# Kernel optimization log

Hardware: AMD Instinct MI355X
Metric: run time of the kernel (lower is better)

## Reference

```python
import jax, jax.numpy as jnp
import numpy as np

B, S, D = 4, 2048, 1024
H = 16
HD = D // H  # 64
MASKED_BIAS = jnp.float32(-10000.0)


def setup_inputs() -> dict:
    key = jax.random.key(0)
    ks = jax.random.split(key, 5)
    std = 0.02
    return {
        "hidden_states": jax.random.normal(ks[0], (B, S, D), jnp.float32),
        "Wq": jax.random.normal(ks[1], (D, D), jnp.float32) * std,
        "bq": jnp.zeros((D,), jnp.float32),
        "Wk": jax.random.normal(ks[2], (D, D), jnp.float32) * std,
        "bk": jnp.zeros((D,), jnp.float32),
        "Wv": jax.random.normal(ks[3], (D, D), jnp.float32) * std,
        "bv": jnp.zeros((D,), jnp.float32),
        "Wo": jax.random.normal(ks[4], (D, D), jnp.float32) * std,
        "bo": jnp.zeros((D,), jnp.float32),
    }


def _split_heads(x):
    # [B, S, D] -> [B, H, S, HD]
    return x.reshape(B, S, H, HD).transpose(0, 2, 1, 3)


def reference(hidden_states, Wq, bq, Wk, bk, Wv, bv, Wo, bo):
    q = _split_heads(hidden_states @ Wq + bq)
    k = _split_heads(hidden_states @ Wk + bk)
    v = _split_heads(hidden_states @ Wv + bv)

    # scores [B, H, S, S], scaled by sqrt(head_dim) (scale=True)
    w = jnp.einsum("bhqd,bhkd->bhqk", q, k) / jnp.sqrt(jnp.float32(HD))
    causal = jnp.tril(jnp.ones((S, S), dtype=bool))  # [S, S]
    w = jnp.where(causal[None, None], w, MASKED_BIAS)
    w = jax.nn.softmax(w, axis=-1)
    # attn_pdrop = 0.0 -> dropout is identity

    a = jnp.einsum("bhqk,bhkd->bhqd", w, v)  # [B, H, S, HD]
    a = a.transpose(0, 2, 1, 3).reshape(B, S, D)  # merge heads
    out = a @ Wo + bo
    # resid_pdrop = 0.0 -> identity
    return out
```

## Files before the change

kernel.cpp:

```cpp
#include <hip/hip_runtime.h>
#include <stdint.h>

typedef unsigned short u16;
typedef __bf16 bf16x8 __attribute__((ext_vector_type(8)));
typedef float f32x4 __attribute__((ext_vector_type(4)));
typedef float f32x16 __attribute__((ext_vector_type(16)));
typedef unsigned int u32x4 __attribute__((ext_vector_type(4)));
typedef u16 u16x8 __attribute__((ext_vector_type(8)));
typedef u16 u16x4 __attribute__((ext_vector_type(4)));

#define MFMA16(a, b, c) __builtin_amdgcn_mfma_f32_16x16x32_bf16((a), (b), (c), 0, 0, 0)
#define MFMA32(a, b, c) __builtin_amdgcn_mfma_f32_32x32x16_bf16((a), (b), (c), 0, 0, 0)

__device__ __forceinline__ u16 f2bf(float f) {
  unsigned u = __float_as_uint(f);
  u += 0x7fff + ((u >> 16) & 1);
  return (u16)(u >> 16);
}

__device__ __forceinline__ unsigned pack_bf2(float lo, float hi) {
  return (unsigned)f2bf(lo) | ((unsigned)f2bf(hi) << 16);
}

__device__ __forceinline__ bf16x8 load_frag(const u16* lds_base, int byteoff) {
  u32x4 v = *(const u32x4*)((const char*)lds_base + byteoff);
  return __builtin_bit_cast(bf16x8, v);
}

#define GLOAD_LDS16(gp, lp)                                                        \
  __builtin_amdgcn_global_load_lds((const __attribute__((address_space(1))) void*)(gp), \
                                   (__attribute__((address_space(3))) void*)(lp), 16, 0, 0)

template <int ROWS>
__device__ __forceinline__ void stage_tile(const u16* __restrict__ src, int ld, u16* lds,
                                           int tid) {
  constexpr int SLOTS = ROWS * 8;
#pragma unroll
  for (int it = 0; it < SLOTS / 256; ++it) {
    const int s = it * 256 + tid;
    const int row = s >> 3;
    const int seg = (s & 7) ^ (row & 7);
    const u16* g = src + row * ld + seg * 8;
    u16* l = lds + (it * 256 + (tid & ~63)) * 8;
    GLOAD_LDS16(g, l);
  }
}


__global__ __launch_bounds__(256) void cvt_x(const float* __restrict__ in,
                                             u16* __restrict__ out) {
  const int i = (int)blockIdx.x * 256 + (int)threadIdx.x;
  const float4 a = ((const float4*)in)[2 * i];
  const float4 b = ((const float4*)in)[2 * i + 1];
  u16x8 o;
  o[0] = f2bf(a.x); o[1] = f2bf(a.y); o[2] = f2bf(a.z); o[3] = f2bf(a.w);
  o[4] = f2bf(b.x); o[5] = f2bf(b.y); o[6] = f2bf(b.z); o[7] = f2bf(b.w);
  ((u16x8*)out)[i] = o;
}

__global__ __launch_bounds__(256) void cvt_w_t(const float* __restrict__ W,
                                               u16* __restrict__ Wt) {
  __shared__ u16 t[64][65];
  const int tid = (int)threadIdx.x;
  const int r = tid >> 2;
  const int cs = (tid & 3) * 16;
  const int tr = (int)blockIdx.y * 64;
  const int tc = (int)blockIdx.x * 64;
#pragma unroll
  for (int i = 0; i < 16; i += 4) {
    const float4 v = *(const float4*)&W[(size_t)(tr + r) * 1024 + tc + cs + i];
    t[r][cs + i + 0] = f2bf(v.x);
    t[r][cs + i + 1] = f2bf(v.y);
    t[r][cs + i + 2] = f2bf(v.z);
    t[r][cs + i + 3] = f2bf(v.w);
  }
  __syncthreads();
  u16 tmp[16];
#pragma unroll
  for (int i = 0; i < 16; ++i) tmp[i] = t[cs + i][r];
  u16x8 o0, o1;
#pragma unroll
  for (int i = 0; i < 8; ++i) { o0[i] = tmp[i]; o1[i] = tmp[8 + i]; }
  *(u16x8*)&Wt[(size_t)(tc + r) * 1024 + tr + cs] = o0;
  *(u16x8*)&Wt[(size_t)(tc + r) * 1024 + tr + cs + 8] = o1;
}


template <int OUT_MODE>
__global__ __launch_bounds__(256) void gemm_bt(const u16* __restrict__ A,
                                               const u16* __restrict__ Bt,
                                               const float* __restrict__ bias,
                                               void* __restrict__ Cout) {
  constexpr int N = 1024, K = 1024;
  __shared__ __align__(16) u16 lds[2 * 128 * 64];
  const int tid = (int)threadIdx.x;
  const int w = tid >> 6, lane = tid & 63;
  const int wm = w >> 1, wn = w & 1;
  const int lr = lane & 15, lg = lane >> 4;
  const int mt = (int)blockIdx.y, nt = (int)blockIdx.x;

  const u16* Abase = A + (size_t)mt * 128 * K;
  const u16* Bbase = Bt + (size_t)nt * 128 * K;

  f32x4 acc[4][4] = {};

  for (int k0 = 0; k0 < K; k0 += 64) {
    stage_tile<128>(Abase + k0, K, lds, tid);
    stage_tile<128>(Bbase + k0, K, lds + 128 * 64, tid);
    __syncthreads();
#pragma unroll
    for (int ks = 0; ks < 2; ++ks) {
      bf16x8 af[4], bf[4];
#pragma unroll
      for (int i = 0; i < 4; ++i) {
        const int ar = wm * 64 + i * 16 + lr;
        af[i] = load_frag(lds, ar * 128 + ((ks * 64 + lg * 16) ^ ((ar & 7) << 4)));
        const int br = wn * 64 + i * 16 + lr;
        bf[i] = load_frag(lds + 128 * 64, br * 128 + ((ks * 64 + lg * 16) ^ ((br & 7) << 4)));
      }
#pragma unroll
      for (int mf = 0; mf < 4; ++mf)
#pragma unroll
        for (int nf = 0; nf < 4; ++nf) acc[mf][nf] = MFMA16(af[mf], bf[nf], acc[mf][nf]);
    }
    __syncthreads();
  }

#pragma unroll
  for (int mf = 0; mf < 4; ++mf) {
#pragma unroll
    for (int nf = 0; nf < 4; ++nf) {
      const int col = nt * 128 + wn * 64 + nf * 16 + lr;
      const float bv = bias[col];
#pragma unroll
      for (int r = 0; r < 4; ++r) {
        const int row = mt * 128 + wm * 64 + mf * 16 + lg * 4 + r;
        const float v = acc[mf][nf][r] + bv;
        if (OUT_MODE == 0) {
          ((u16*)Cout)[(size_t)row * N + col] = f2bf(v);
        } else if (OUT_MODE == 1) {
          ((float*)Cout)[(size_t)row * N + col] = v;
        } else if (OUT_MODE == 2) {
          const int b = row >> 11, s = row & 2047;
          const int h = col >> 6, d = col & 63;
          const size_t addr = ((size_t)((b * 16 + h) * 32 + (s >> 6))) * 4096 +
                              (size_t)(d >> 5) * 2048 + (size_t)((s & 63) >> 4) * 512 +
                              (size_t)((d & 31) | (((s >> 3) & 1) << 5)) * 8 + (s & 7);
          ((u16*)Cout)[addr] = f2bf(v);
        } else {
          const int b = row >> 11, s = row & 2047;
          const int h = col >> 6, d = col & 63;
          const size_t addr = ((size_t)((b * 16 + h) * 64 + (s >> 5))) * 2048 +
                              (size_t)(d >> 4) * 512 +
                              (size_t)((s & 31) | (((d >> 3) & 1) << 5)) * 8 + (d & 7);
          ((u16*)Cout)[addr] = f2bf(v);
        }
      }
    }
  }
}


template <int MASKED>
__device__ __forceinline__ void attn_tile(const u16* __restrict__ kp,
                                          const u16* __restrict__ vp,
                                          const bf16x8 (&qf)[4], const int hi,
                                          const int tmask, f32x16& o0, f32x16& o1,
                                          float& m_run, float& l_run) {
  bf16x8 kf[2][4], vf[2][4];
#pragma unroll
  for (int sb = 0; sb < 2; ++sb)
#pragma unroll
    for (int dk = 0; dk < 4; ++dk)
      kf[sb][dk] = *(const bf16x8*)(kp + sb * 2048 + dk * 512);
#pragma unroll
  for (int db = 0; db < 2; ++db)
#pragma unroll
    for (int ks = 0; ks < 4; ++ks)
      vf[db][ks] = *(const bf16x8*)(vp + db * 2048 + ks * 512);

  f32x16 p0 = {}, p1 = {};
#pragma unroll
  for (int dk = 0; dk < 4; ++dk) {
    p0 = MFMA32(kf[0][dk], qf[dk], p0);
    p1 = MFMA32(kf[1][dk], qf[dk], p1);
  }

  float mx = -3.0e38f;
#pragma unroll
  for (int r = 0; r < 16; ++r) {
    if (MASKED) {
      const int kl = (r & 3) + 8 * (r >> 2) + 4 * hi;
      if (kl > tmask) p0[r] = -1.0e30f;
      if (kl + 32 > tmask) p1[r] = -1.0e30f;
    }
    mx = fmaxf(mx, fmaxf(p0[r], p1[r]));
  }
  mx = fmaxf(mx, __shfl_xor(mx, 32));

  if (__any(mx > m_run + 64.0f)) {
    const float mnew = fmaxf(m_run, mx);
    const float alpha = __expf((m_run - mnew) * 0.125f);
    m_run = mnew;
    l_run *= alpha;
#pragma unroll
    for (int r = 0; r < 16; ++r) { o0[r] *= alpha; o1[r] *= alpha; }
  }

  float rs = 0.0f;
#pragma unroll
  for (int r = 0; r < 16; ++r) {
    p0[r] = __expf((p0[r] - m_run) * 0.125f);
    p1[r] = __expf((p1[r] - m_run) * 0.125f);
    rs += p0[r] + p1[r];
  }
  rs += __shfl_xor(rs, 32);
  l_run += rs;

  unsigned c[16];
#pragma unroll
  for (int r2 = 0; r2 < 8; ++r2) {
    c[r2] = pack_bf2(p0[2 * r2], p0[2 * r2 + 1]);
    c[8 + r2] = pack_bf2(p1[2 * r2], p1[2 * r2 + 1]);
  }
  bf16x8 pf[4];
#pragma unroll
  for (int ks = 0; ks < 4; ++ks) {
    const int base = (ks >> 1) * 8 + (ks & 1) * 4;
    const unsigned x = __shfl_xor(hi ? c[base + 0] : c[base + 2], 32);
    const unsigned y = __shfl_xor(hi ? c[base + 1] : c[base + 3], 32);
    u32x4 wv;
    wv[0] = hi ? x : c[base + 0];
    wv[1] = hi ? y : c[base + 1];
    wv[2] = hi ? c[base + 2] : x;
    wv[3] = hi ? c[base + 3] : y;
    pf[ks] = __builtin_bit_cast(bf16x8, wv);
  }

#pragma unroll
  for (int ks = 0; ks < 4; ++ks) {
    o0 = MFMA32(vf[0][ks], pf[ks], o0);
    o1 = MFMA32(vf[1][ks], pf[ks], o1);
  }
}

__global__ __launch_bounds__(256) void attn_fwd(const u16* __restrict__ Qb,
                                                const u16* __restrict__ Kf,
                                                const u16* __restrict__ Vf,
                                                u16* __restrict__ Ab) {
  const int tid = (int)threadIdx.x;
  const int w = tid >> 6, lane = tid & 63;
  const int ln = lane & 31, hi = lane >> 5;

  const int id = (int)blockIdx.x;
  const int xcd = id & 7, slot = id >> 3;
  const int bh = (xcd << 3) | (slot & 7);
  const int qt = 15 - (slot >> 3);
  const int b = bh >> 4, h = bh & 15;
  const int wq = qt * 128 + w * 32;
  const int qrow = wq + ln;

  const u16* qp = Qb + (size_t)(b * 2048 + qrow) * 1024 + h * 64 + hi * 8;
  bf16x8 qf[4];
#pragma unroll
  for (int dk = 0; dk < 4; ++dk) qf[dk] = *(const bf16x8*)(qp + dk * 16);

  const u16* kp = Kf + (size_t)bh * 131072 + lane * 8;
  const u16* vp = Vf + (size_t)bh * 131072 + lane * 8;

  f32x16 o0 = {}, o1 = {};
  float m_run = -3.0e38f, l_run = 0.0f;

  const int nfull = (wq + 1) >> 6;
  for (int j = 0; j < nfull; ++j)
    attn_tile<0>(kp + (size_t)j * 4096, vp + (size_t)j * 4096, qf, hi, 0, o0, o1, m_run, l_run);
  attn_tile<1>(kp + (size_t)nfull * 4096, vp + (size_t)nfull * 4096, qf, hi,
               qrow - nfull * 64, o0, o1, m_run, l_run);

  const float inv = 1.0f / l_run;
  u16* op = Ab + (size_t)(b * 2048 + qrow) * 1024 + h * 64;
#pragma unroll
  for (int rr = 0; rr < 4; ++rr) {
    u16x4 s0v, s1v;
#pragma unroll
    for (int cc = 0; cc < 4; ++cc) {
      s0v[cc] = f2bf(o0[rr * 4 + cc] * inv);
      s1v[cc] = f2bf(o1[rr * 4 + cc] * inv);
    }
    *(u16x4*)(op + rr * 8 + hi * 4) = s0v;
    *(u16x4*)(op + 32 + rr * 8 + hi * 4) = s1v;
  }
}


extern "C" void kernel_launch(void* const* d_in, const int* in_sizes, int n_in, void* d_out,
                              int out_size, void* d_ws, size_t ws_size, hipStream_t stream) {
  const float* X = (const float*)d_in[0];
  const float* Wq = (const float*)d_in[1];
  const float* bq = (const float*)d_in[2];
  const float* Wk = (const float*)d_in[3];
  const float* bk = (const float*)d_in[4];
  const float* Wv = (const float*)d_in[5];
  const float* bv = (const float*)d_in[6];
  const float* Wo = (const float*)d_in[7];
  const float* bo = (const float*)d_in[8];
  float* out = (float*)d_out;

  u16* ws = (u16*)d_ws;
  u16* Xb = ws;
  u16* Wqt = Xb + 8388608;
  u16* Wkt = Wqt + 1048576;
  u16* Wvt = Wkt + 1048576;
  u16* Wot = Wvt + 1048576;
  u16* Qb = Wot + 1048576;
  u16* Kf = Qb + 8388608;
  u16* Vf = Kf + 8388608;
  u16* Ab = Vf + 8388608;

  cvt_x<<<4096, 256, 0, stream>>>(X, Xb);
  dim3 wtg(16, 16);
  cvt_w_t<<<wtg, 256, 0, stream>>>(Wq, Wqt);
  cvt_w_t<<<wtg, 256, 0, stream>>>(Wk, Wkt);
  cvt_w_t<<<wtg, 256, 0, stream>>>(Wv, Wvt);
  cvt_w_t<<<wtg, 256, 0, stream>>>(Wo, Wot);

  dim3 gg(8, 64);
  gemm_bt<0><<<gg, 256, 0, stream>>>(Xb, Wqt, bq, Qb);
  gemm_bt<3><<<gg, 256, 0, stream>>>(Xb, Wkt, bk, Kf);
  gemm_bt<2><<<gg, 256, 0, stream>>>(Xb, Wvt, bv, Vf);

  attn_fwd<<<1024, 256, 0, stream>>>(Qb, Kf, Vf, Ab);

  gemm_bt<1><<<gg, 256, 0, stream>>>(Ab, Wot, bo, out);
}
```

Measured before the change: 202.5 us.

## Fold softmax scale into Q, use exp2, hardware bf16 pack, permlane swap

Pre-scales Q by log2(e)/sqrt(64) in the projection epilogue so the attention inner loop can use exp2 with no per-element multiply, and adjusts the lazy-rescale threshold to the new units. Replaces the manual round-to-nearest bf16 conversion with native bf16 casts so the compiler can emit packed conversion instructions. Replaces the xor-shuffle plus selects for exchanging P fragments between wave halves with permlane32_swap. Changes the causal query-tile schedule to a zig-zag ordering that interleaves heavy and light tiles for load balance.

```diff
diff --git a/kernel.cpp b/kernel.cpp
--- a/kernel.cpp
+++ b/kernel.cpp
@@ -2,6 +2,7 @@
 #include <stdint.h>
 
 typedef unsigned short u16;
+typedef __bf16 bf16x2 __attribute__((ext_vector_type(2)));
 typedef __bf16 bf16x8 __attribute__((ext_vector_type(8)));
 typedef float f32x4 __attribute__((ext_vector_type(4)));
 typedef float f32x16 __attribute__((ext_vector_type(16)));
@@ -12,14 +13,17 @@
 #define MFMA16(a, b, c) __builtin_amdgcn_mfma_f32_16x16x32_bf16((a), (b), (c), 0, 0, 0)
 #define MFMA32(a, b, c) __builtin_amdgcn_mfma_f32_32x32x16_bf16((a), (b), (c), 0, 0, 0)
 
+#define QSCALE 0.18033688011112042f
+
 __device__ __forceinline__ u16 f2bf(float f) {
-  unsigned u = __float_as_uint(f);
-  u += 0x7fff + ((u >> 16) & 1);
-  return (u16)(u >> 16);
-}
-
-__device__ __forceinline__ unsigned pack_bf2(float lo, float hi) {
-  return (unsigned)f2bf(lo) | ((unsigned)f2bf(hi) << 16);
+  return __builtin_bit_cast(u16, (__bf16)f);
+}
+
+__device__ __forceinline__ unsigned cvtpk(float lo, float hi) {
+  bf16x2 t;
+  t[0] = (__bf16)lo;
+  t[1] = (__bf16)hi;
+  return __builtin_bit_cast(unsigned, t);
 }
 
 __device__ __forceinline__ bf16x8 load_frag(const u16* lds_base, int byteoff) {
@@ -137,7 +141,7 @@
         const int row = mt * 128 + wm * 64 + mf * 16 + lg * 4 + r;
         const float v = acc[mf][nf][r] + bv;
         if (OUT_MODE == 0) {
-          ((u16*)Cout)[(size_t)row * N + col] = f2bf(v);
+          ((u16*)Cout)[(size_t)row * N + col] = f2bf(v * QSCALE);
         } else if (OUT_MODE == 1) {
           ((float*)Cout)[(size_t)row * N + col] = v;
         } else if (OUT_MODE == 2) {
@@ -198,9 +202,9 @@
   }
   mx = fmaxf(mx, __shfl_xor(mx, 32));
 
-  if (__any(mx > m_run + 64.0f)) {
+  if (__any(mx > m_run + 11.5416f)) {
     const float mnew = fmaxf(m_run, mx);
-    const float alpha = __expf((m_run - mnew) * 0.125f);
+    const float alpha = exp2f(m_run - mnew);
     m_run = mnew;
     l_run *= alpha;
 #pragma unroll
@@ -210,8 +214,8 @@
   float rs = 0.0f;
 #pragma unroll
   for (int r = 0; r < 16; ++r) {
-    p0[r] = __expf((p0[r] - m_run) * 0.125f);
-    p1[r] = __expf((p1[r] - m_run) * 0.125f);
+    p0[r] = exp2f(p0[r] - m_run);
+    p1[r] = exp2f(p1[r] - m_run);
     rs += p0[r] + p1[r];
   }
   rs += __shfl_xor(rs, 32);
@@ -219,21 +223,21 @@
 
   unsigned c[16];
 #pragma unroll
-  for (int r2 = 0; r2 < 8; ++r2) {
-    c[r2] = pack_bf2(p0[2 * r2], p0[2 * r2 + 1]);
-    c[8 + r2] = pack_bf2(p1[2 * r2], p1[2 * r2 + 1]);
+  for (int j = 0; j < 8; ++j) {
+    c[j] = cvtpk(p0[2 * j], p0[2 * j + 1]);
+    c[8 + j] = cvtpk(p1[2 * j], p1[2 * j + 1]);
   }
   bf16x8 pf[4];
 #pragma unroll
   for (int ks = 0; ks < 4; ++ks) {
     const int base = (ks >> 1) * 8 + (ks & 1) * 4;
-    const unsigned x = __shfl_xor(hi ? c[base + 0] : c[base + 2], 32);
-    const unsigned y = __shfl_xor(hi ? c[base + 1] : c[base + 3], 32);
+    auto s0 = __builtin_amdgcn_permlane32_swap(c[base + 0], c[base + 2], false, false);
+    auto s1 = __builtin_amdgcn_permlane32_swap(c[base + 1], c[base + 3], false, false);
     u32x4 wv;
-    wv[0] = hi ? x : c[base + 0];
-    wv[1] = hi ? y : c[base + 1];
-    wv[2] = hi ? c[base + 2] : x;
-    wv[3] = hi ? c[base + 3] : y;
+    wv[0] = s0[0];
+    wv[1] = s1[0];
+    wv[2] = s0[1];
+    wv[3] = s1[1];
     pf[ks] = __builtin_bit_cast(bf16x8, wv);
   }
 
@@ -255,7 +259,8 @@
   const int id = (int)blockIdx.x;
   const int xcd = id & 7, slot = id >> 3;
   const int bh = (xcd << 3) | (slot & 7);
-  const int qt = 15 - (slot >> 3);
+  static const int qtmap[16] = {15, 14, 13, 12, 0, 1, 2, 3, 11, 10, 9, 8, 4, 5, 6, 7};
+  const int qt = qtmap[slot >> 3];
   const int b = bh >> 4, h = bh & 15;
   const int wq = qt * 128 + w * 32;
   const int qrow = wq + ln;
```

New measurement: 215.1 us. +6.3%, slower.
